# Kernel optimization log

Measured on AMD Instinct MI355X. Metric: run time of the kernel, lower is better.

Reference implementation:

```python
import jax, jax.numpy as jnp
import numpy as np

A = 100000          # num atoms
E = 1600000         # num edges
N_SPECIES = 4       # len(atomic_types)
N_RADIAL = 8        # l=1 radial functions (max_radial hyper)
N_PSEUDO = 4        # Alchemical pseudo species
D = N_RADIAL * N_PSEUDO  # embedding_dim = 32
RC = 5.0            # cutoff radius
WIDTH = 0.5         # shifted-cosine width


def setup_inputs() -> dict:
    key = jax.random.key(0)
    ks = jax.random.split(key, 9)
    return {
        "interatomic_vectors": jax.random.normal(ks[0], (E, 3), dtype=jnp.float32),
        "centers": jax.random.randint(ks[1], (E,), 0, A),
        "neighbors": jax.random.randint(ks[2], (E,), 0, A),
        "species": jax.random.randint(ks[3], (A,), 0, N_SPECIES),
        "structures": jnp.sort(jax.random.randint(ks[4], (A,), 0, 64)),
        "atom_index_in_structure": jax.random.randint(ks[5], (A,), 0, A),
        # learned params
        "W_alch": jax.random.normal(ks[6], (N_SPECIES, N_PSEUDO), dtype=jnp.float32) * 0.1,
        "center_embedding": jax.random.normal(ks[7], (N_SPECIES, D), dtype=jnp.float32),
        "W_contract": jax.random.normal(ks[8], (3, D), dtype=jnp.float32) * (1.0 / np.sqrt(D)),
    }


def _shifted_cosine(d):
    # 1 below rc-width, smooth cosine taper to 0 at rc
    inner = RC - WIDTH
    taper = 0.5 * (jnp.cos(jnp.pi * (d - inner) / WIDTH) + 1.0)
    return jnp.where(d < inner, 1.0, jnp.where(d < RC, taper, 0.0))


def reference(interatomic_vectors, centers, neighbors, species, structures,
              atom_index_in_structure, W_alch, center_embedding, W_contract):
    eps = 1e-12
    d = jnp.sqrt(jnp.sum(interatomic_vectors * interatomic_vectors, axis=1) + eps)  # (E,)
    fc = _shifted_cosine(d)                                                         # (E,)
    # Laplacian-eigenstate-style l=1 radial basis: sin(n*pi*d/rc)/d, n=1..N_RADIAL
    n = jnp.arange(1, N_RADIAL + 1, dtype=jnp.float32)
    R = jnp.sin(n[None, :] * (jnp.pi / RC) * d[:, None]) / d[:, None]               # (E, nR)
    # real l=1 spherical harmonics, m order (-1, 0, 1) -> (y, z, x)/d
    Y = interatomic_vectors[:, jnp.array([1, 2, 0])] / d[:, None]                   # (E, 3)
    # alchemical pseudo-species weights of the neighbor
    alch = W_alch[species[neighbors]]                                               # (E, nQ)
    # per-edge expansion coefficients, scattered onto centers
    edge = (fc[:, None, None, None]
            * Y[:, :, None, None]
            * R[:, None, :, None]
            * alch[:, None, None, :])                                               # (E, 3, nR, nQ)
    spex = jax.ops.segment_sum(edge, centers, num_segments=A)                       # (A, 3, nR, nQ)
    x = spex.reshape(A, 3, D)                                                       # reshape(n,q -> n*q)
    x = x * center_embedding[species][:, None, :]                                   # center encoding
    out = jnp.einsum("amd,od->amo", x, W_contract)                                  # (A, 3, 3)
    return out
```

## Files before the change

### kernel.cpp

```cpp
#include <hip/hip_runtime.h>
#include <hip/hip_fp16.h>


constexpr int NSP  = 4;
constexpr int NRAD = 8;
constexpr int NPS  = 4;
constexpr int DDIM = NRAD * NPS;

constexpr int APB      = 512;
constexpr int APB_SH   = 9;
constexpr int NBIN_MAX = 256;
constexpr int SPLIT    = 4;
constexpr int PH1_BLK  = 512;
constexpr int PH1_U    = 4;
constexpr int PH1_REC  = PH1_BLK * PH1_U;
constexpr int CAP2     = 3072;

__device__ __forceinline__ unsigned pack2(float a, float b) {
    union { __half2 h; unsigned u; } cv;
    cv.h = __floats2half2_rn(a, b);
    return cv.u;
}
__device__ __forceinline__ float2 unpack2(unsigned u) {
    union { unsigned u; __half2 h; } cv;
    cv.u = u;
    return __half22float2(cv.h);
}

__device__ __forceinline__ void build_w2(
    float* sW2, const float* cemb, const float* Wc, const float* W_alch,
    int tid, int nthreads)
{
    for (int i = tid; i < 3 * NRAD * 16; i += nthreads) {
        int p  = i & 15;
        int n  = (i >> 4) & 7;
        int o  = i >> 7;
        int sc = p >> 2, sn = p & 3;
        float w = 0.0f;
        #pragma unroll
        for (int q = 0; q < NPS; q++)
            w += cemb[sc * DDIM + n * NPS + q] * Wc[o * DDIM + n * NPS + q]
               * W_alch[sn * NPS + q];
        sW2[i] = w;
    }
}

__device__ __forceinline__ bool edge_math(
    float vx, float vy, float vz, int pair, const float* sW2,
    float g[3], float t[3])
{
    float d2    = vx * vx + vy * vy + vz * vz + 1e-12f;
    float d     = sqrtf(d2);
    float inv_d = 1.0f / d;

    const float PI = 3.14159265358979323846f;
    const float RCUT = 5.0f, INNER = 4.5f, INVW = 2.0f;
    if (d >= RCUT) return false;
    float taper = 0.5f * (cosf(PI * (d - INNER) * INVW) + 1.0f);
    float fc = (d < INNER) ? 1.0f : taper;

    float theta = (PI / RCUT) * d;
    float s1 = sinf(theta);
    float c1 = cosf(theta);
    float two_c = 2.0f * c1;
    float R[NRAD];
    R[0] = s1 * inv_d;
    float sm2 = 0.0f, sm1 = s1;
    #pragma unroll
    for (int n = 1; n < NRAD; n++) {
        float s = two_c * sm1 - sm2;
        sm2 = sm1; sm1 = s;
        R[n] = s * inv_d;
    }

    #pragma unroll
    for (int o = 0; o < 3; o++) {
        float acc = 0.0f;
        #pragma unroll
        for (int n = 0; n < NRAD; n++)
            acc += R[n] * sW2[(o * NRAD + n) * 16 + pair];
        t[o] = acc;
    }
    g[0] = fc * vy * inv_d;
    g[1] = fc * vz * inv_d;
    g[2] = fc * vx * inv_d;
    return true;
}

__device__ __forceinline__ void atomic_spill(float* out, int c,
                                             int ry, int rz, int rw)
{
    float2 g01 = unpack2((unsigned)ry);
    float2 g2t = unpack2((unsigned)rz);
    float2 t12 = unpack2((unsigned)rw);
    float g[3] = { g01.x, g01.y, g2t.x };
    float t[3] = { g2t.y, t12.x, t12.y };
    float* op = out + (size_t)c * 9;
    #pragma unroll
    for (int m = 0; m < 3; m++)
        #pragma unroll
        for (int o = 0; o < 3; o++)
            atomicAdd(op + m * 3 + o, g[m] * t[o]);
}

__global__ __launch_bounds__(PH1_BLK) void vb_phase1(
    const float* __restrict__ vecs,
    const int*   __restrict__ centers,
    const int*   __restrict__ neighbors,
    const int*   __restrict__ species,
    const float* __restrict__ W_alch,
    const float* __restrict__ cemb,
    const float* __restrict__ Wc,
    int*         __restrict__ gcursor,
    int4*        __restrict__ payload,
    float*       __restrict__ out,
    int E, int cap)
{
    __shared__ float sW2[3 * NRAD * 16];
    __shared__ int4  srec[PH1_REC];
    __shared__ int lcount[NBIN_MAX], lscan[NBIN_MAX], lexcl[NBIN_MAX],
                   lbase[NBIN_MAX], lcur[NBIN_MAX];

    int tid = threadIdx.x;
    build_w2(sW2, cemb, Wc, W_alch, tid, PH1_BLK);
    for (int i = tid; i < NBIN_MAX; i += PH1_BLK) lcount[i] = 0;
    __syncthreads();

    int4 rec[PH1_U];
    #pragma unroll
    for (int u = 0; u < PH1_U; u++) {
        int e = blockIdx.x * PH1_REC + u * PH1_BLK + tid;
        rec[u].x = -1;
        if (e < E) {
            float vx = vecs[3 * e + 0];
            float vy = vecs[3 * e + 1];
            float vz = vecs[3 * e + 2];
            int c  = centers[e];
            int pair = species[c] * 4 + species[neighbors[e]];
            float g[3], t[3];
            if (edge_math(vx, vy, vz, pair, sW2, g, t)) {
                rec[u].x = c;
                rec[u].y = (int)pack2(g[0], g[1]);
                rec[u].z = (int)pack2(g[2], t[0]);
                rec[u].w = (int)pack2(t[1], t[2]);
                atomicAdd(&lcount[c >> APB_SH], 1);
            }
        }
    }
    __syncthreads();

    if (tid < NBIN_MAX) lscan[tid] = lcount[tid];
    __syncthreads();
    for (int off = 1; off < NBIN_MAX; off <<= 1) {
        int v = 0;
        if (tid < NBIN_MAX) {
            v = lscan[tid];
            if (tid >= off) v += lscan[tid - off];
        }
        __syncthreads();
        if (tid < NBIN_MAX) lscan[tid] = v;
        __syncthreads();
    }
    if (tid < NBIN_MAX) {
        int ex = lscan[tid] - lcount[tid];
        lexcl[tid] = ex;
        lcur[tid]  = ex;
        int n = lcount[tid];
        lbase[tid] = n ? atomicAdd(&gcursor[tid], n) : 0;
    }
    __syncthreads();

    #pragma unroll
    for (int u = 0; u < PH1_U; u++) {
        if (rec[u].x >= 0) {
            int bin = rec[u].x >> APB_SH;
            int p = atomicAdd(&lcur[bin], 1);
            srec[p] = rec[u];
        }
    }
    __syncthreads();

    int total = lscan[NBIN_MAX - 1];
    for (int i = tid; i < total; i += PH1_BLK) {
        int4 r = srec[i];
        int bin  = r.x >> APB_SH;
        int slot = lbase[bin] + (i - lexcl[bin]);
        if (slot < cap)
            payload[(size_t)bin * cap + slot] = r;
        else
            atomic_spill(out, r.x, r.y, r.z, r.w);
    }
}

__global__ __launch_bounds__(256) void vb_phase2(
    const int*  __restrict__ gcursor,
    const int4* __restrict__ payload,
    float*      __restrict__ partial,
    float*      __restrict__ out,
    int out_elems, int cap)
{
    __shared__ int4 srec2[CAP2];
    __shared__ unsigned short sidx[CAP2];
    __shared__ int cnt[APB], cscan[APB], ccur[APB];

    int b = blockIdx.x / SPLIT;
    int s = blockIdx.x % SPLIT;
    int tid = threadIdx.x;

    for (int i = tid; i < APB; i += 256) cnt[i] = 0;
    __syncthreads();

    int count = min(gcursor[b], cap);
    int lo = (int)(((long)count * s) / SPLIT);
    int hi = (int)(((long)count * (s + 1)) / SPLIT);
    int n  = hi - lo;
    int nc = min(n, CAP2);
    const int4* pb = payload + (size_t)b * cap + lo;

    for (int i = tid; i < nc; i += 256) {
        int4 r = pb[i];
        srec2[i] = r;
        atomicAdd(&cnt[r.x & (APB - 1)], 1);
    }
    __syncthreads();

    cscan[tid] = cnt[tid];
    cscan[tid + 256] = cnt[tid + 256];
    __syncthreads();
    for (int off = 1; off < APB; off <<= 1) {
        int i0 = tid, i1 = tid + 256;
        int v0 = cscan[i0]; if (i0 >= off) v0 += cscan[i0 - off];
        int v1 = cscan[i1]; if (i1 >= off) v1 += cscan[i1 - off];
        __syncthreads();
        cscan[i0] = v0;
        cscan[i1] = v1;
        __syncthreads();
    }
    ccur[tid] = cscan[tid] - cnt[tid];
    ccur[tid + 256] = cscan[tid + 256] - cnt[tid + 256];
    __syncthreads();

    for (int i = tid; i < nc; i += 256) {
        int a = srec2[i].x & (APB - 1);
        int p = atomicAdd(&ccur[a], 1);
        sidx[p] = (unsigned short)i;
    }
    __syncthreads();

    for (int a = tid; a < APB; a += 256) {
        int en = cscan[a];
        int st = en - cnt[a];
        float acc[9] = {0,0,0,0,0,0,0,0,0};
        for (int j = st; j < en; j++) {
            int4 r = srec2[sidx[j]];
            float2 g01 = unpack2((unsigned)r.y);
            float2 g2t = unpack2((unsigned)r.z);
            float2 t12 = unpack2((unsigned)r.w);
            float g0 = g01.x, g1 = g01.y, g2 = g2t.x;
            float t0 = g2t.y, t1 = t12.x, t2 = t12.y;
            acc[0] += g0 * t0; acc[1] += g0 * t1; acc[2] += g0 * t2;
            acc[3] += g1 * t0; acc[4] += g1 * t1; acc[5] += g1 * t2;
            acc[6] += g2 * t0; acc[7] += g2 * t1; acc[8] += g2 * t2;
        }
        size_t gi = ((size_t)(b << APB_SH) + a) * 9;
        if (gi < (size_t)out_elems) {
            float* pd = partial + (size_t)s * out_elems + gi;
            #pragma unroll
            for (int k = 0; k < 9; k++) pd[k] = acc[k];
        }
    }

    for (int i = CAP2 + tid; i < n; i += 256) {
        int4 r = pb[i];
        atomic_spill(out, r.x, r.y, r.z, r.w);
    }
}

__global__ __launch_bounds__(256) void vb_reduce(
    const float* __restrict__ partial, float* __restrict__ out, int n)
{
    int i = blockIdx.x * blockDim.x + threadIdx.x;
    if (i >= n) return;
    out[i] += partial[i] + partial[(size_t)n + i]
            + partial[2 * (size_t)n + i] + partial[3 * (size_t)n + i];
}

__global__ __launch_bounds__(256) void vb_edge_fallback(
    const float* __restrict__ vecs,
    const int*   __restrict__ centers,
    const int*   __restrict__ neighbors,
    const int*   __restrict__ species,
    const float* __restrict__ W_alch,
    const float* __restrict__ cemb,
    const float* __restrict__ Wc,
    float*       __restrict__ out,
    int E)
{
    __shared__ float sW2[3 * NRAD * 16];
    build_w2(sW2, cemb, Wc, W_alch, threadIdx.x, blockDim.x);
    __syncthreads();

    int e = blockIdx.x * blockDim.x + threadIdx.x;
    if (e >= E) return;
    float vx = vecs[3 * e + 0], vy = vecs[3 * e + 1], vz = vecs[3 * e + 2];
    int c = centers[e];
    int pair = species[c] * 4 + species[neighbors[e]];
    float g[3], t[3];
    if (!edge_math(vx, vy, vz, pair, sW2, g, t)) return;
    float* op = out + (size_t)c * 9;
    #pragma unroll
    for (int m = 0; m < 3; m++)
        #pragma unroll
        for (int o = 0; o < 3; o++)
            atomicAdd(op + m * 3 + o, g[m] * t[o]);
}

extern "C" void kernel_launch(void* const* d_in, const int* in_sizes, int n_in,
                              void* d_out, int out_size, void* d_ws, size_t ws_size,
                              hipStream_t stream) {
    const float* vecs      = (const float*)d_in[0];
    const int*   centers   = (const int*)d_in[1];
    const int*   neighbors = (const int*)d_in[2];
    const int*   species   = (const int*)d_in[3];
    const float* W_alch    = (const float*)d_in[6];
    const float* cemb      = (const float*)d_in[7];
    const float* Wc        = (const float*)d_in[8];
    float*       out       = (float*)d_out;

    int E = in_sizes[1];
    int A = in_sizes[3];
    int nbin = (A + APB - 1) >> APB_SH;

    size_t out_bytes = (size_t)out_size * sizeof(float);
    long cap = 0;
    long fixed = 4096 + (long)SPLIT * out_bytes;
    if ((long)ws_size > fixed) {
        cap = ((long)ws_size - fixed) / 16 / nbin;
        cap &= ~7L;
        if (cap > 16384) cap = 16384;
    }
    long mean = (long)E / nbin + 1;

    hipMemsetAsync(d_out, 0, out_bytes, stream);

    if (nbin <= NBIN_MAX && cap >= mean + mean / 16) {
        int*   gcursor = (int*)d_ws;
        int4*  payload = (int4*)((char*)d_ws + 4096);
        float* partial = (float*)((char*)d_ws + 4096 + (size_t)nbin * cap * 16);
        hipMemsetAsync(d_ws, 0, 4096, stream);

        int g1 = (E + PH1_REC - 1) / PH1_REC;
        vb_phase1<<<g1, PH1_BLK, 0, stream>>>(vecs, centers, neighbors, species,
                                              W_alch, cemb, Wc,
                                              gcursor, payload, out, E, (int)cap);
        vb_phase2<<<nbin * SPLIT, 256, 0, stream>>>(gcursor, payload, partial,
                                                    out, out_size, (int)cap);
        int rg = (out_size + 255) / 256;
        vb_reduce<<<rg, 256, 0, stream>>>(partial, out, out_size);
    } else {
        int grid = (E + 255) / 256;
        vb_edge_fallback<<<grid, 256, 0, stream>>>(vecs, centers, neighbors, species,
                                                   W_alch, cemb, Wc, out, E);
    }
}
```

Before: 145.8 us.

## Replace shared-atomic binning with wave ballot ranking and fuse split reduction

Both phases now compute each record's bin rank with wavefront ballots and per-wave histograms instead of shared-memory atomics. The multi-barrier Hillis-Steele scans are replaced by a single-wave shuffle scan. The separate reduce kernel is removed: the last of the SPLIT blocks for each bin, found through a global done counter, sums the partials into the output. This cuts barriers, LDS atomic contention and one kernel launch, at the cost of more ballot instructions and a threadfence-based completion protocol.

```diff
diff --git a/kernel.cpp b/kernel.cpp
--- a/kernel.cpp
+++ b/kernel.cpp
@@ -15,6 +15,8 @@
 constexpr int PH1_U    = 4;
 constexpr int PH1_REC  = PH1_BLK * PH1_U;
 constexpr int CAP2     = 3072;
+constexpr int IT2_MAX  = CAP2 / 256;
+constexpr int PBSZ     = APB * 9;
 
 __device__ __forceinline__ unsigned pack2(float a, float b) {
     union { __half2 h; unsigned u; } cv;
@@ -101,6 +103,17 @@
         #pragma unroll
         for (int o = 0; o < 3; o++)
             atomicAdd(op + m * 3 + o, g[m] * t[o]);
+}
+
+template <int NB>
+__device__ __forceinline__ unsigned long long key_mask(int key, bool valid) {
+    unsigned long long m = __ballot(valid);
+    #pragma unroll
+    for (int bit = 0; bit < NB; bit++) {
+        unsigned long long b = __ballot((key >> bit) & 1);
+        m &= ((key >> bit) & 1) ? b : ~b;
+    }
+    return m;
 }
 
 __global__ __launch_bounds__(PH1_BLK) void vb_phase1(
@@ -118,69 +131,97 @@
 {
     __shared__ float sW2[3 * NRAD * 16];
     __shared__ int4  srec[PH1_REC];
-    __shared__ int lcount[NBIN_MAX], lscan[NBIN_MAX], lexcl[NBIN_MAX],
-                   lbase[NBIN_MAX], lcur[NBIN_MAX];
-
-    int tid = threadIdx.x;
+    __shared__ int   whist[8][NBIN_MAX];
+    __shared__ __align__(16) int lcols[NBIN_MAX];
+    __shared__ int   lexcl[NBIN_MAX];
+    __shared__ int   lbase[NBIN_MAX];
+    __shared__ int   sTotal;
+
+    int tid  = threadIdx.x;
+    int w    = tid >> 6;
+    int lane = tid & 63;
+    unsigned long long lt = ((unsigned long long)1 << lane) - 1;
+
     build_w2(sW2, cemb, Wc, W_alch, tid, PH1_BLK);
-    for (int i = tid; i < NBIN_MAX; i += PH1_BLK) lcount[i] = 0;
+    for (int i = tid; i < 8 * NBIN_MAX; i += PH1_BLK) ((int*)whist)[i] = 0;
     __syncthreads();
 
     int4 rec[PH1_U];
+    int  keyv[PH1_U], rk[PH1_U];
+
     #pragma unroll
     for (int u = 0; u < PH1_U; u++) {
         int e = blockIdx.x * PH1_REC + u * PH1_BLK + tid;
-        rec[u].x = -1;
+        bool valid = false;
+        int c = 0;
         if (e < E) {
             float vx = vecs[3 * e + 0];
             float vy = vecs[3 * e + 1];
             float vz = vecs[3 * e + 2];
-            int c  = centers[e];
+            c = centers[e];
             int pair = species[c] * 4 + species[neighbors[e]];
             float g[3], t[3];
             if (edge_math(vx, vy, vz, pair, sW2, g, t)) {
-                rec[u].x = c;
+                valid = true;
                 rec[u].y = (int)pack2(g[0], g[1]);
                 rec[u].z = (int)pack2(g[2], t[0]);
                 rec[u].w = (int)pack2(t[1], t[2]);
-                atomicAdd(&lcount[c >> APB_SH], 1);
             }
         }
-    }
-    __syncthreads();
-
-    if (tid < NBIN_MAX) lscan[tid] = lcount[tid];
-    __syncthreads();
-    for (int off = 1; off < NBIN_MAX; off <<= 1) {
-        int v = 0;
-        if (tid < NBIN_MAX) {
-            v = lscan[tid];
-            if (tid >= off) v += lscan[tid - off];
-        }
-        __syncthreads();
-        if (tid < NBIN_MAX) lscan[tid] = v;
-        __syncthreads();
-    }
+        rec[u].x = valid ? c : -1;
+        int key = valid ? (c >> APB_SH) : 0;
+        keyv[u] = key;
+        unsigned long long m = key_mask<8>(key, valid);
+        int rank = (int)__popcll(m & lt);
+        int prev = valid ? whist[w][key] : 0;
+        if (valid && rank == 0)
+            whist[w][key] = prev + (int)__popcll(m);
+        rk[u] = prev + rank;
+    }
+    __syncthreads();
+
     if (tid < NBIN_MAX) {
-        int ex = lscan[tid] - lcount[tid];
-        lexcl[tid] = ex;
-        lcur[tid]  = ex;
-        int n = lcount[tid];
-        lbase[tid] = n ? atomicAdd(&gcursor[tid], n) : 0;
+        int run = 0;
+        #pragma unroll
+        for (int w2 = 0; w2 < 8; w2++) {
+            int v = whist[w2][tid];
+            whist[w2][tid] = run;
+            run += v;
+        }
+        lcols[tid] = run;
+        lbase[tid] = run ? atomicAdd(&gcursor[tid], run) : 0;
+    }
+    __syncthreads();
+
+    if (tid < 64) {
+        int4 v = *(const int4*)&lcols[tid * 4];
+        int s0 = v.x, s1 = s0 + v.y, s2 = s1 + v.z, s3 = s2 + v.w;
+        int incl = s3;
+        #pragma unroll
+        for (int off = 1; off < 64; off <<= 1) {
+            int t = __shfl_up(incl, off, 64);
+            if (tid >= off) incl += t;
+        }
+        int ex = incl - s3;
+        lexcl[tid * 4 + 0] = ex;
+        lexcl[tid * 4 + 1] = ex + s0;
+        lexcl[tid * 4 + 2] = ex + s1;
+        lexcl[tid * 4 + 3] = ex + s2;
+        if (tid == 63) sTotal = incl;
     }
     __syncthreads();
 
     #pragma unroll
     for (int u = 0; u < PH1_U; u++) {
         if (rec[u].x >= 0) {
-            int bin = rec[u].x >> APB_SH;
-            int p = atomicAdd(&lcur[bin], 1);
-            srec[p] = rec[u];
-        }
-    }
-    __syncthreads();
-
-    int total = lscan[NBIN_MAX - 1];
+            int key = keyv[u];
+            int slot = lexcl[key] + whist[w][key] + rk[u];
+            srec[slot] = rec[u];
+        }
+    }
+    __syncthreads();
+
+    int total = sTotal;
     for (int i = tid; i < total; i += PH1_BLK) {
         int4 r = srec[i];
         int bin  = r.x >> APB_SH;
@@ -196,18 +237,25 @@
     const int*  __restrict__ gcursor,
     const int4* __restrict__ payload,
     float*      __restrict__ partial,
+    int*        __restrict__ done,
     float*      __restrict__ out,
     int out_elems, int cap)
 {
     __shared__ int4 srec2[CAP2];
     __shared__ unsigned short sidx[CAP2];
-    __shared__ int cnt[APB], cscan[APB], ccur[APB];
+    __shared__ int whist2[SPLIT][APB];
+    __shared__ __align__(16) int acnt[APB];
+    __shared__ int aexcl[APB];
+    __shared__ int sFlag;
 
     int b = blockIdx.x / SPLIT;
     int s = blockIdx.x % SPLIT;
-    int tid = threadIdx.x;
-
-    for (int i = tid; i < APB; i += 256) cnt[i] = 0;
+    int tid  = threadIdx.x;
+    int w    = tid >> 6;
+    int lane = tid & 63;
+    unsigned long long lt = ((unsigned long long)1 << lane) - 1;
+
+    for (int i = tid; i < SPLIT * APB; i += 256) ((int*)whist2)[i] = 0;
     __syncthreads();
 
     int count = min(gcursor[b], cap);
@@ -217,39 +265,71 @@
     int nc = min(n, CAP2);
     const int4* pb = payload + (size_t)b * cap + lo;
 
-    for (int i = tid; i < nc; i += 256) {
-        int4 r = pb[i];
-        srec2[i] = r;
-        atomicAdd(&cnt[r.x & (APB - 1)], 1);
-    }
-    __syncthreads();
-
-    cscan[tid] = cnt[tid];
-    cscan[tid + 256] = cnt[tid + 256];
-    __syncthreads();
-    for (int off = 1; off < APB; off <<= 1) {
-        int i0 = tid, i1 = tid + 256;
-        int v0 = cscan[i0]; if (i0 >= off) v0 += cscan[i0 - off];
-        int v1 = cscan[i1]; if (i1 >= off) v1 += cscan[i1 - off];
-        __syncthreads();
-        cscan[i0] = v0;
-        cscan[i1] = v1;
-        __syncthreads();
-    }
-    ccur[tid] = cscan[tid] - cnt[tid];
-    ccur[tid + 256] = cscan[tid + 256] - cnt[tid + 256];
-    __syncthreads();
-
-    for (int i = tid; i < nc; i += 256) {
-        int a = srec2[i].x & (APB - 1);
-        int p = atomicAdd(&ccur[a], 1);
-        sidx[p] = (unsigned short)i;
+    int iters = (nc + 255) >> 8;
+    int keyv[IT2_MAX], rk2[IT2_MAX];
+
+    for (int k = 0; k < iters; k++) {
+        int i = k * 256 + tid;
+        bool valid = i < nc;
+        int key = 0;
+        if (valid) {
+            int4 r = pb[i];
+            srec2[i] = r;
+            key = r.x & (APB - 1);
+        }
+        keyv[k] = key;
+        unsigned long long m = key_mask<9>(key, valid);
+        int rank = (int)__popcll(m & lt);
+        int prev = valid ? whist2[w][key] : 0;
+        if (valid && rank == 0)
+            whist2[w][key] = prev + (int)__popcll(m);
+        rk2[k] = prev + rank;
     }
     __syncthreads();
 
     for (int a = tid; a < APB; a += 256) {
-        int en = cscan[a];
-        int st = en - cnt[a];
+        int run = 0;
+        #pragma unroll
+        for (int w2 = 0; w2 < SPLIT; w2++) {
+            int v = whist2[w2][a];
+            whist2[w2][a] = run;
+            run += v;
+        }
+        acnt[a] = run;
+    }
+    __syncthreads();
+
+    if (tid < 64) {
+        int base = tid * 8;
+        int pre[8];
+        int sum = 0;
+        #pragma unroll
+        for (int j = 0; j < 8; j++) { pre[j] = sum; sum += acnt[base + j]; }
+        int incl = sum;
+        #pragma unroll
+        for (int off = 1; off < 64; off <<= 1) {
+            int t = __shfl_up(incl, off, 64);
+            if (tid >= off) incl += t;
+        }
+        int ex = incl - sum;
+        #pragma unroll
+        for (int j = 0; j < 8; j++) aexcl[base + j] = ex + pre[j];
+    }
+    __syncthreads();
+
+    for (int k = 0; k < iters; k++) {
+        int i = k * 256 + tid;
+        if (i < nc) {
+            int key = keyv[k];
+            int slot = aexcl[key] + whist2[w][key] + rk2[k];
+            sidx[slot] = (unsigned short)i;
+        }
+    }
+    __syncthreads();
+
+    float* pdst = partial + ((size_t)b * SPLIT + s) * PBSZ;
+    for (int a = tid; a < APB; a += 256) {
+        int st = aexcl[a], en = st + acnt[a];
         float acc[9] = {0,0,0,0,0,0,0,0,0};
         for (int j = st; j < en; j++) {
             int4 r = srec2[sidx[j]];
@@ -262,27 +342,34 @@
             acc[3] += g1 * t0; acc[4] += g1 * t1; acc[5] += g1 * t2;
             acc[6] += g2 * t0; acc[7] += g2 * t1; acc[8] += g2 * t2;
         }
-        size_t gi = ((size_t)(b << APB_SH) + a) * 9;
-        if (gi < (size_t)out_elems) {
-            float* pd = partial + (size_t)s * out_elems + gi;
-            #pragma unroll
-            for (int k = 0; k < 9; k++) pd[k] = acc[k];
-        }
+        #pragma unroll
+        for (int kk = 0; kk < 9; kk++) pdst[a * 9 + kk] = acc[kk];
     }
 
     for (int i = CAP2 + tid; i < n; i += 256) {
         int4 r = pb[i];
         atomic_spill(out, r.x, r.y, r.z, r.w);
     }
-}
-
-__global__ __launch_bounds__(256) void vb_reduce(
-    const float* __restrict__ partial, float* __restrict__ out, int n)
-{
-    int i = blockIdx.x * blockDim.x + threadIdx.x;
-    if (i >= n) return;
-    out[i] += partial[i] + partial[(size_t)n + i]
-            + partial[2 * (size_t)n + i] + partial[3 * (size_t)n + i];
+
+    __threadfence();
+    __syncthreads();
+    if (tid == 0) sFlag = atomicAdd(&done[b], 1);
+    __syncthreads();
+    if (sFlag == SPLIT - 1) {
+        __threadfence();
+        size_t ob = ((size_t)b << APB_SH) * 9;
+        const float* psrc = partial + (size_t)b * SPLIT * PBSZ;
+        for (int i = tid; i < PBSZ; i += 256) {
+            size_t gi = ob + i;
+            if (gi < (size_t)out_elems) {
+                float v = out[gi];
+                #pragma unroll
+                for (int s2 = 0; s2 < SPLIT; s2++)
+                    v += psrc[(size_t)s2 * PBSZ + i];
+                out[gi] = v;
+            }
+        }
+    }
 }
 
 __global__ __launch_bounds__(256) void vb_edge_fallback(
@@ -331,9 +418,9 @@
     int A = in_sizes[3];
     int nbin = (A + APB - 1) >> APB_SH;
 
-    size_t out_bytes = (size_t)out_size * sizeof(float);
+    size_t part_bytes = (size_t)nbin * SPLIT * PBSZ * sizeof(float);
     long cap = 0;
-    long fixed = 4096 + (long)SPLIT * out_bytes;
+    long fixed = 4096 + (long)part_bytes;
     if ((long)ws_size > fixed) {
         cap = ((long)ws_size - fixed) / 16 / nbin;
         cap &= ~7L;
@@ -341,10 +428,11 @@
     }
     long mean = (long)E / nbin + 1;
 
-    hipMemsetAsync(d_out, 0, out_bytes, stream);
+    hipMemsetAsync(d_out, 0, (size_t)out_size * sizeof(float), stream);
 
     if (nbin <= NBIN_MAX && cap >= mean + mean / 16) {
         int*   gcursor = (int*)d_ws;
+        int*   done    = (int*)((char*)d_ws + 2048);
         int4*  payload = (int4*)((char*)d_ws + 4096);
         float* partial = (float*)((char*)d_ws + 4096 + (size_t)nbin * cap * 16);
         hipMemsetAsync(d_ws, 0, 4096, stream);
@@ -354,9 +442,7 @@
                                               W_alch, cemb, Wc,
                                               gcursor, payload, out, E, (int)cap);
         vb_phase2<<<nbin * SPLIT, 256, 0, stream>>>(gcursor, payload, partial,
-                                                    out, out_size, (int)cap);
-        int rg = (out_size + 255) / 256;
-        vb_reduce<<<rg, 256, 0, stream>>>(partial, out, out_size);
+                                                    done, out, out_size, (int)cap);
     } else {
         int grid = (E + 255) / 256;
         vb_edge_fallback<<<grid, 256, 0, stream>>>(vecs, centers, neighbors, species,
```

After: 313.1 us. +114.7%, slower.

## Replace LDS atomics in phase2 counting sort with wave-ballot match and warp-scan

Applied to the files above, without the earlier changes.

Phase 2's per-atom counting sort previously used shared-memory atomicAdd for histogramming and slot assignment, plus an 18-barrier Hillis-Steele scan over 512 bins. It now uses ballot-based key matching per 64-lane wave, so one leader per key updates a per-wave histogram without atomics. The 512-bin prefix is computed by a single wave with shuffle scans. The stable, deterministic ordering comes at the cost of nine extra ballots per element per pass and more shared memory.

```diff
diff --git a/kernel.cpp b/kernel.cpp
--- a/kernel.cpp
+++ b/kernel.cpp
@@ -11,6 +11,7 @@
 constexpr int APB_SH   = 9;
 constexpr int NBIN_MAX = 256;
 constexpr int SPLIT    = 4;
+constexpr int NW2      = 4;
 constexpr int PH1_BLK  = 512;
 constexpr int PH1_U    = 4;
 constexpr int PH1_REC  = PH1_BLK * PH1_U;
@@ -101,6 +102,17 @@
         #pragma unroll
         for (int o = 0; o < 3; o++)
             atomicAdd(op + m * 3 + o, g[m] * t[o]);
+}
+
+template <int NB>
+__device__ __forceinline__ unsigned long long key_mask(int key, bool valid) {
+    unsigned long long m = __ballot(valid);
+    #pragma unroll
+    for (int bit = 0; bit < NB; bit++) {
+        unsigned long long b = __ballot((key >> bit) & 1);
+        m &= ((key >> bit) & 1) ? b : ~b;
+    }
+    return m;
 }
 
 __global__ __launch_bounds__(PH1_BLK) void vb_phase1(
@@ -201,13 +213,18 @@
 {
     __shared__ int4 srec2[CAP2];
     __shared__ unsigned short sidx[CAP2];
-    __shared__ int cnt[APB], cscan[APB], ccur[APB];
+    __shared__ int whist2[NW2][APB];
+    __shared__ __align__(16) int acnt[APB];
+    __shared__ int aexcl[APB];
 
     int b = blockIdx.x / SPLIT;
     int s = blockIdx.x % SPLIT;
-    int tid = threadIdx.x;
-
-    for (int i = tid; i < APB; i += 256) cnt[i] = 0;
+    int tid  = threadIdx.x;
+    int w    = tid >> 6;
+    int lane = tid & 63;
+    unsigned long long lt = ((unsigned long long)1 << lane) - 1;
+
+    for (int i = tid; i < NW2 * APB; i += 256) ((int*)whist2)[i] = 0;
     __syncthreads();
 
     int count = min(gcursor[b], cap);
@@ -217,39 +234,69 @@
     int nc = min(n, CAP2);
     const int4* pb = payload + (size_t)b * cap + lo;
 
-    for (int i = tid; i < nc; i += 256) {
-        int4 r = pb[i];
-        srec2[i] = r;
-        atomicAdd(&cnt[r.x & (APB - 1)], 1);
-    }
-    __syncthreads();
-
-    cscan[tid] = cnt[tid];
-    cscan[tid + 256] = cnt[tid + 256];
-    __syncthreads();
-    for (int off = 1; off < APB; off <<= 1) {
-        int i0 = tid, i1 = tid + 256;
-        int v0 = cscan[i0]; if (i0 >= off) v0 += cscan[i0 - off];
-        int v1 = cscan[i1]; if (i1 >= off) v1 += cscan[i1 - off];
-        __syncthreads();
-        cscan[i0] = v0;
-        cscan[i1] = v1;
-        __syncthreads();
-    }
-    ccur[tid] = cscan[tid] - cnt[tid];
-    ccur[tid + 256] = cscan[tid + 256] - cnt[tid + 256];
-    __syncthreads();
-
-    for (int i = tid; i < nc; i += 256) {
-        int a = srec2[i].x & (APB - 1);
-        int p = atomicAdd(&ccur[a], 1);
-        sidx[p] = (unsigned short)i;
+    for (int i0 = 0; i0 < nc; i0 += 256) {
+        int i = i0 + tid;
+        bool valid = i < nc;
+        int key = 0;
+        if (valid) {
+            int4 r = pb[i];
+            srec2[i] = r;
+            key = r.x & (APB - 1);
+        }
+        unsigned long long m = key_mask<9>(key, valid);
+        int rank = (int)__popcll(m & lt);
+        int prev = valid ? whist2[w][key] : 0;
+        if (valid && rank == 0)
+            whist2[w][key] = prev + (int)__popcll(m);
     }
     __syncthreads();
 
     for (int a = tid; a < APB; a += 256) {
-        int en = cscan[a];
-        int st = en - cnt[a];
+        int run = 0;
+        #pragma unroll
+        for (int w2 = 0; w2 < NW2; w2++) {
+            int v = whist2[w2][a];
+            whist2[w2][a] = run;
+            run += v;
+        }
+        acnt[a] = run;
+    }
+    __syncthreads();
+
+    if (tid < 64) {
+        int base = tid * 8;
+        int pre[8];
+        int sum = 0;
+        #pragma unroll
+        for (int j = 0; j < 8; j++) { pre[j] = sum; sum += acnt[base + j]; }
+        int incl = sum;
+        #pragma unroll
+        for (int off = 1; off < 64; off <<= 1) {
+            int t = __shfl_up(incl, off, 64);
+            if (tid >= off) incl += t;
+        }
+        int ex = incl - sum;
+        #pragma unroll
+        for (int j = 0; j < 8; j++) aexcl[base + j] = ex + pre[j];
+    }
+    __syncthreads();
+
+    for (int i0 = 0; i0 < nc; i0 += 256) {
+        int i = i0 + tid;
+        bool valid = i < nc;
+        int key = valid ? (srec2[i].x & (APB - 1)) : 0;
+        unsigned long long m = key_mask<9>(key, valid);
+        int rank = (int)__popcll(m & lt);
+        int prev = valid ? whist2[w][key] : 0;
+        if (valid && rank == 0)
+            whist2[w][key] = prev + (int)__popcll(m);
+        if (valid)
+            sidx[aexcl[key] + prev + rank] = (unsigned short)i;
+    }
+    __syncthreads();
+
+    for (int a = tid; a < APB; a += 256) {
+        int st = aexcl[a], en = st + acnt[a];
         float acc[9] = {0,0,0,0,0,0,0,0,0};
         for (int j = st; j < en; j++) {
             int4 r = srec2[sidx[j]];
```

Measured after the change: 156.3 us. 7.2% more time.

## Shrink bins to 128 atoms, drop split partials and reduce kernel, add overflow buffer

Applied to the files above, without the earlier changes.

Bins shrink from 512 to 128 atoms, giving about 782 bins with one phase-2 block each. Each block loops over its bin's records in shared-memory chunks and writes its final outputs directly, so the SPLIT partial buffers, the reduce kernel and the output memset are gone. Overflow records now go to a global overflow list that every phase-2 block scans, replacing atomic spills. Local scans use wavefront shuffles instead of barrier-based Hillis-Steele. The risk is that many records overflow, which would make every block scan a long list serially; the cap is also limited to 4096 per bin.

```diff
diff --git a/kernel.cpp b/kernel.cpp
--- a/kernel.cpp
+++ b/kernel.cpp
@@ -7,14 +7,14 @@
 constexpr int NPS  = 4;
 constexpr int DDIM = NRAD * NPS;
 
-constexpr int APB      = 512;
-constexpr int APB_SH   = 9;
-constexpr int NBIN_MAX = 256;
-constexpr int SPLIT    = 4;
+constexpr int APB      = 128;
+constexpr int APB_SH   = 7;
+constexpr int NBIN_PAD = 832;
 constexpr int PH1_BLK  = 512;
 constexpr int PH1_U    = 4;
 constexpr int PH1_REC  = PH1_BLK * PH1_U;
-constexpr int CAP2     = 3072;
+constexpr int CAP2     = 2560;
+constexpr int OVF_CAP  = 65536;
 
 __device__ __forceinline__ unsigned pack2(float a, float b) {
     union { __half2 h; unsigned u; } cv;
@@ -85,22 +85,6 @@
     g[1] = fc * vz * inv_d;
     g[2] = fc * vx * inv_d;
     return true;
-}
-
-__device__ __forceinline__ void atomic_spill(float* out, int c,
-                                             int ry, int rz, int rw)
-{
-    float2 g01 = unpack2((unsigned)ry);
-    float2 g2t = unpack2((unsigned)rz);
-    float2 t12 = unpack2((unsigned)rw);
-    float g[3] = { g01.x, g01.y, g2t.x };
-    float t[3] = { g2t.y, t12.x, t12.y };
-    float* op = out + (size_t)c * 9;
-    #pragma unroll
-    for (int m = 0; m < 3; m++)
-        #pragma unroll
-        for (int o = 0; o < 3; o++)
-            atomicAdd(op + m * 3 + o, g[m] * t[o]);
 }
 
 __global__ __launch_bounds__(PH1_BLK) void vb_phase1(
@@ -112,18 +96,20 @@
     const float* __restrict__ cemb,
     const float* __restrict__ Wc,
     int*         __restrict__ gcursor,
+    int*         __restrict__ ovfcnt,
+    int4*        __restrict__ ovf,
     int4*        __restrict__ payload,
-    float*       __restrict__ out,
-    int E, int cap)
+    int E, int nbin, int cap)
 {
     __shared__ float sW2[3 * NRAD * 16];
     __shared__ int4  srec[PH1_REC];
-    __shared__ int lcount[NBIN_MAX], lscan[NBIN_MAX], lexcl[NBIN_MAX],
-                   lbase[NBIN_MAX], lcur[NBIN_MAX];
+    __shared__ int lcount[NBIN_PAD], lexcl[NBIN_PAD],
+                   lbase[NBIN_PAD], lcur[NBIN_PAD];
+    __shared__ int sTotal;
 
     int tid = threadIdx.x;
     build_w2(sW2, cemb, Wc, W_alch, tid, PH1_BLK);
-    for (int i = tid; i < NBIN_MAX; i += PH1_BLK) lcount[i] = 0;
+    for (int i = tid; i < NBIN_PAD; i += PH1_BLK) lcount[i] = 0;
     __syncthreads();
 
     int4 rec[PH1_U];
@@ -149,24 +135,29 @@
     }
     __syncthreads();
 
-    if (tid < NBIN_MAX) lscan[tid] = lcount[tid];
-    __syncthreads();
-    for (int off = 1; off < NBIN_MAX; off <<= 1) {
-        int v = 0;
-        if (tid < NBIN_MAX) {
-            v = lscan[tid];
-            if (tid >= off) v += lscan[tid - off];
-        }
-        __syncthreads();
-        if (tid < NBIN_MAX) lscan[tid] = v;
-        __syncthreads();
-    }
-    if (tid < NBIN_MAX) {
-        int ex = lscan[tid] - lcount[tid];
-        lexcl[tid] = ex;
-        lcur[tid]  = ex;
-        int n = lcount[tid];
-        lbase[tid] = n ? atomicAdd(&gcursor[tid], n) : 0;
+    if (tid < 64) {
+        int base = tid * 13;
+        int pre[13];
+        int sum = 0;
+        #pragma unroll
+        for (int j = 0; j < 13; j++) { pre[j] = sum; sum += lcount[base + j]; }
+        int incl = sum;
+        #pragma unroll
+        for (int off = 1; off < 64; off <<= 1) {
+            int t = __shfl_up(incl, off, 64);
+            if (tid >= off) incl += t;
+        }
+        int ex = incl - sum;
+        #pragma unroll
+        for (int j = 0; j < 13; j++) lexcl[base + j] = ex + pre[j];
+        if (tid == 63) sTotal = incl;
+    }
+    __syncthreads();
+
+    for (int i = tid; i < nbin; i += PH1_BLK) {
+        lcur[i] = lexcl[i];
+        int n = lcount[i];
+        lbase[i] = n ? atomicAdd(&gcursor[i], n) : 0;
     }
     __syncthreads();
 
@@ -180,79 +171,97 @@
     }
     __syncthreads();
 
-    int total = lscan[NBIN_MAX - 1];
+    int total = sTotal;
     for (int i = tid; i < total; i += PH1_BLK) {
         int4 r = srec[i];
         int bin  = r.x >> APB_SH;
         int slot = lbase[bin] + (i - lexcl[bin]);
-        if (slot < cap)
+        if (slot < cap) {
             payload[(size_t)bin * cap + slot] = r;
-        else
-            atomic_spill(out, r.x, r.y, r.z, r.w);
+        } else {
+            int p = atomicAdd(ovfcnt, 1);
+            if (p < OVF_CAP) ovf[p] = r;
+        }
     }
 }
 
 __global__ __launch_bounds__(256) void vb_phase2(
     const int*  __restrict__ gcursor,
+    const int*  __restrict__ ovfcnt,
+    const int4* __restrict__ ovf,
     const int4* __restrict__ payload,
-    float*      __restrict__ partial,
     float*      __restrict__ out,
-    int out_elems, int cap)
+    int A, int cap)
 {
     __shared__ int4 srec2[CAP2];
     __shared__ unsigned short sidx[CAP2];
-    __shared__ int cnt[APB], cscan[APB], ccur[APB];
-
-    int b = blockIdx.x / SPLIT;
-    int s = blockIdx.x % SPLIT;
+    __shared__ int cnt[APB], aexcl[APB], ccur[APB];
+    __shared__ float sout[APB * 9];
+
+    int b   = blockIdx.x;
     int tid = threadIdx.x;
-
-    for (int i = tid; i < APB; i += 256) cnt[i] = 0;
-    __syncthreads();
-
     int count = min(gcursor[b], cap);
-    int lo = (int)(((long)count * s) / SPLIT);
-    int hi = (int)(((long)count * (s + 1)) / SPLIT);
-    int n  = hi - lo;
-    int nc = min(n, CAP2);
-    const int4* pb = payload + (size_t)b * cap + lo;
-
-    for (int i = tid; i < nc; i += 256) {
-        int4 r = pb[i];
-        srec2[i] = r;
-        atomicAdd(&cnt[r.x & (APB - 1)], 1);
-    }
-    __syncthreads();
-
-    cscan[tid] = cnt[tid];
-    cscan[tid + 256] = cnt[tid + 256];
-    __syncthreads();
-    for (int off = 1; off < APB; off <<= 1) {
-        int i0 = tid, i1 = tid + 256;
-        int v0 = cscan[i0]; if (i0 >= off) v0 += cscan[i0 - off];
-        int v1 = cscan[i1]; if (i1 >= off) v1 += cscan[i1 - off];
-        __syncthreads();
-        cscan[i0] = v0;
-        cscan[i1] = v1;
-        __syncthreads();
-    }
-    ccur[tid] = cscan[tid] - cnt[tid];
-    ccur[tid + 256] = cscan[tid + 256] - cnt[tid + 256];
-    __syncthreads();
-
-    for (int i = tid; i < nc; i += 256) {
-        int a = srec2[i].x & (APB - 1);
-        int p = atomicAdd(&ccur[a], 1);
-        sidx[p] = (unsigned short)i;
-    }
-    __syncthreads();
-
-    for (int a = tid; a < APB; a += 256) {
-        int en = cscan[a];
-        int st = en - cnt[a];
-        float acc[9] = {0,0,0,0,0,0,0,0,0};
-        for (int j = st; j < en; j++) {
-            int4 r = srec2[sidx[j]];
+    const int4* pb = payload + (size_t)b * cap;
+
+    float acc[9] = {0,0,0,0,0,0,0,0,0};
+    int myatom = (b << APB_SH) + tid;
+
+    for (int base = 0; base < count; base += CAP2) {
+        int nc = min(count - base, CAP2);
+        if (tid < APB) cnt[tid] = 0;
+        __syncthreads();
+
+        for (int i = tid; i < nc; i += 256) {
+            int4 r = pb[base + i];
+            srec2[i] = r;
+            atomicAdd(&cnt[r.x & (APB - 1)], 1);
+        }
+        __syncthreads();
+
+        if (tid < 64) {
+            int c0 = cnt[2 * tid], c1 = cnt[2 * tid + 1];
+            int s1 = c0 + c1;
+            int incl = s1;
+            #pragma unroll
+            for (int off = 1; off < 64; off <<= 1) {
+                int t = __shfl_up(incl, off, 64);
+                if (tid >= off) incl += t;
+            }
+            int ex = incl - s1;
+            aexcl[2 * tid]     = ex;
+            aexcl[2 * tid + 1] = ex + c0;
+        }
+        __syncthreads();
+        if (tid < APB) ccur[tid] = aexcl[tid];
+        __syncthreads();
+
+        for (int i = tid; i < nc; i += 256) {
+            int k = srec2[i].x & (APB - 1);
+            sidx[atomicAdd(&ccur[k], 1)] = (unsigned short)i;
+        }
+        __syncthreads();
+
+        if (tid < APB) {
+            int st = aexcl[tid], en = st + cnt[tid];
+            for (int j = st; j < en; j++) {
+                int4 r = srec2[sidx[j]];
+                float2 g01 = unpack2((unsigned)r.y);
+                float2 g2t = unpack2((unsigned)r.z);
+                float2 t12 = unpack2((unsigned)r.w);
+                float g0 = g01.x, g1 = g01.y, g2 = g2t.x;
+                float t0 = g2t.y, t1 = t12.x, t2 = t12.y;
+                acc[0] += g0 * t0; acc[1] += g0 * t1; acc[2] += g0 * t2;
+                acc[3] += g1 * t0; acc[4] += g1 * t1; acc[5] += g1 * t2;
+                acc[6] += g2 * t0; acc[7] += g2 * t1; acc[8] += g2 * t2;
+            }
+        }
+        __syncthreads();
+    }
+
+    int novf = min(*ovfcnt, OVF_CAP);
+    for (int i = 0; i < novf; i++) {
+        int4 r = ovf[i];
+        if (tid < APB && r.x == myatom) {
             float2 g01 = unpack2((unsigned)r.y);
             float2 g2t = unpack2((unsigned)r.z);
             float2 t12 = unpack2((unsigned)r.w);
@@ -262,27 +271,19 @@
             acc[3] += g1 * t0; acc[4] += g1 * t1; acc[5] += g1 * t2;
             acc[6] += g2 * t0; acc[7] += g2 * t1; acc[8] += g2 * t2;
         }
-        size_t gi = ((size_t)(b << APB_SH) + a) * 9;
-        if (gi < (size_t)out_elems) {
-            float* pd = partial + (size_t)s * out_elems + gi;
-            #pragma unroll
-            for (int k = 0; k < 9; k++) pd[k] = acc[k];
-        }
-    }
-
-    for (int i = CAP2 + tid; i < n; i += 256) {
-        int4 r = pb[i];
-        atomic_spill(out, r.x, r.y, r.z, r.w);
-    }
-}
-
-__global__ __launch_bounds__(256) void vb_reduce(
-    const float* __restrict__ partial, float* __restrict__ out, int n)
-{
-    int i = blockIdx.x * blockDim.x + threadIdx.x;
-    if (i >= n) return;
-    out[i] += partial[i] + partial[(size_t)n + i]
-            + partial[2 * (size_t)n + i] + partial[3 * (size_t)n + i];
+    }
+
+    if (tid < APB) {
+        #pragma unroll
+        for (int k = 0; k < 9; k++) sout[tid * 9 + k] = acc[k];
+    }
+    __syncthreads();
+    size_t gbase = (size_t)b * APB * 9;
+    size_t lim = (size_t)A * 9;
+    for (int i = tid; i < APB * 9; i += 256) {
+        size_t gi = gbase + i;
+        if (gi < lim) out[gi] = sout[i];
+    }
 }
 
 __global__ __launch_bounds__(256) void vb_edge_fallback(
@@ -331,33 +332,32 @@
     int A = in_sizes[3];
     int nbin = (A + APB - 1) >> APB_SH;
 
-    size_t out_bytes = (size_t)out_size * sizeof(float);
+    size_t ovf_off = 4096;
+    size_t pay_off = ovf_off + (size_t)OVF_CAP * 16;
     long cap = 0;
-    long fixed = 4096 + (long)SPLIT * out_bytes;
-    if ((long)ws_size > fixed) {
-        cap = ((long)ws_size - fixed) / 16 / nbin;
+    if (ws_size > pay_off) {
+        cap = (long)((ws_size - pay_off) / 16) / nbin;
         cap &= ~7L;
-        if (cap > 16384) cap = 16384;
+        if (cap > 4096) cap = 4096;
     }
     long mean = (long)E / nbin + 1;
 
-    hipMemsetAsync(d_out, 0, out_bytes, stream);
-
-    if (nbin <= NBIN_MAX && cap >= mean + mean / 16) {
-        int*   gcursor = (int*)d_ws;
-        int4*  payload = (int4*)((char*)d_ws + 4096);
-        float* partial = (float*)((char*)d_ws + 4096 + (size_t)nbin * cap * 16);
+    if (nbin <= NBIN_PAD && nbin <= 3840 / 4 && cap >= mean + mean / 8) {
+        int*  gcursor = (int*)d_ws;
+        int*  ovfcnt  = (int*)((char*)d_ws + 3840);
+        int4* ovf     = (int4*)((char*)d_ws + ovf_off);
+        int4* payload = (int4*)((char*)d_ws + pay_off);
         hipMemsetAsync(d_ws, 0, 4096, stream);
 
         int g1 = (E + PH1_REC - 1) / PH1_REC;
         vb_phase1<<<g1, PH1_BLK, 0, stream>>>(vecs, centers, neighbors, species,
                                               W_alch, cemb, Wc,
-                                              gcursor, payload, out, E, (int)cap);
-        vb_phase2<<<nbin * SPLIT, 256, 0, stream>>>(gcursor, payload, partial,
-                                                    out, out_size, (int)cap);
-        int rg = (out_size + 255) / 256;
-        vb_reduce<<<rg, 256, 0, stream>>>(partial, out, out_size);
+                                              gcursor, ovfcnt, ovf, payload,
+                                              E, nbin, (int)cap);
+        vb_phase2<<<nbin, 256, 0, stream>>>(gcursor, ovfcnt, ovf, payload,
+                                            out, A, (int)cap);
     } else {
+        hipMemsetAsync(d_out, 0, (size_t)out_size * sizeof(float), stream);
         int grid = (E + 255) / 256;
         vb_edge_fallback<<<grid, 256, 0, stream>>>(vecs, centers, neighbors, species,
                                                    W_alch, cemb, Wc, out, E);
```

Result: no change. 144.2 us (-1.1%).
